# Performance work log

Measured on AMD Instinct MI355X. Metric: run time of the kernel, lower is better.

The kernel has to match this reference:

```python
import jax, jax.numpy as jnp
import numpy as np

COMMIT_W = 0.25
ENT_W = 0.1
ENT_T = 0.01
EPS = 1e-5


def setup_inputs() -> dict:
    key = jax.random.key(0)
    kx, kc = jax.random.split(key)
    x = jax.random.normal(kx, (32, 32, 32, 256), dtype=jnp.float32)
    # variance_scaling(1.0, fan_in, uniform) -> U(-sqrt(3/fan_in), sqrt(3/fan_in)), fan_in = 256
    lim = float(np.sqrt(3.0 / 256.0))
    codebook = jax.random.uniform(kc, (1024, 256), dtype=jnp.float32, minval=-lim, maxval=lim)
    return {"x": x, "codebook": codebook}


def _cdist(flat, codebook):
    # Euclidean distance (with sqrt, as jnp.linalg.norm in the original),
    # computed via the expanded quadratic form to avoid the [N,K,D] intermediate.
    d2 = (jnp.sum(flat * flat, axis=-1, keepdims=True)
          + jnp.sum(codebook * codebook, axis=-1)[None, :]
          - 2.0 * (flat @ codebook.T))
    return jnp.sqrt(jnp.maximum(d2, 0.0))  # [N, K]


def reference(x, codebook):
    D = x.shape[-1]
    flat = x.reshape(-1, D)                      # [N, D]
    distances = _cdist(flat, codebook)           # [N, K]
    flat_indices = jnp.argmin(distances, axis=-1)  # [N]
    indices = flat_indices.reshape(x.shape[:-1])
    # one_hot(indices) @ codebook == gather
    quantized = codebook[flat_indices].reshape(x.shape)

    # optax.l2_loss = 0.5 * (pred - target)^2
    commit_loss = 0.5 * jnp.mean((x - jax.lax.stop_gradient(quantized)) ** 2) * COMMIT_W
    codebook_loss = 0.5 * jnp.mean((jax.lax.stop_gradient(x) - quantized) ** 2)

    # entropy loss on affinity = -distances
    logits = (-distances) / ENT_T                # [N, K]
    probs = jax.nn.softmax(logits, axis=-1)
    log_probs = jax.nn.log_softmax(logits + EPS, axis=-1)
    avg_probs = jnp.mean(probs, axis=0)          # [K]
    avg_entropy = -jnp.sum(avg_probs * jnp.log(avg_probs + EPS))
    sample_entropy = -jnp.mean(jnp.sum(probs * log_probs, axis=-1))
    entropy_loss = (sample_entropy - avg_entropy) * ENT_W

    vq_loss = codebook_loss + commit_loss + entropy_loss
    # straight-through estimator
    quantized_st = x + jax.lax.stop_gradient(quantized - x)
    return quantized_st, vq_loss, commit_loss, codebook_loss, entropy_loss, indices
```

## Files before the change

### kernel.cpp

```cpp
#include <hip/hip_runtime.h>

#define N_ROWS 32768
#define DIMS 256
#define K_CODES 1024
#define MT 64
#define NCHUNK 256
#define KC 16
#define SA 68
#define SB 260

static constexpr size_t SC_OFF  = 8388608;
static constexpr size_t IDX_OFF = 8388612;

__device__ inline float wsum64(float v){
  #pragma unroll
  for(int off=32; off; off>>=1) v += __shfl_xor(v, off, 64);
  return v;
}

__global__ __launch_bounds__(256) void rowsq_np512_kernel(const float* __restrict__ X,
                                                          const float* __restrict__ CB,
                                                          float* __restrict__ xsq,
                                                          float* __restrict__ csq){
  const int t = threadIdx.x;
  const int wv = t >> 6, l = t & 63;
  const int sub = l >> 4, li = l & 15;
  #pragma unroll
  for(int p=0; p<4; p++){
    int r = blockIdx.x*64 + p*16 + wv*4 + sub;
    const float* s0; float* dst;
    if(r < K_CODES){ s0 = CB + (size_t)r*DIMS; dst = csq + r; }
    else { s0 = X + (size_t)(r - K_CODES)*DIMS; dst = xsq + (r - K_CODES); }
    float blk[2];
    #pragma unroll
    for(int bb=0; bb<2; bb++){
      float q[8];
      #pragma unroll
      for(int j=0;j<8;j++){
        float a = s0[bb*128 + j*16 + li];
        q[j] = __fmul_rn(a, a);
      }
      float v = __fadd_rn(__fadd_rn(__fadd_rn(q[0],q[1]), __fadd_rn(q[2],q[3])),
                          __fadd_rn(__fadd_rn(q[4],q[5]), __fadd_rn(q[6],q[7])));
      v = __fadd_rn(v, __shfl_xor(v, 8, 64));
      v = __fadd_rn(v, __shfl_xor(v, 4, 64));
      v = __fadd_rn(v, __shfl_xor(v, 2, 64));
      v = __fadd_rn(v, __shfl_xor(v, 1, 64));
      blk[bb] = v;
    }
    if(li == 0) *dst = __fadd_rn(blk[0], blk[1]);
  }
}

__global__ __launch_bounds__(256,2) void fused_argmin_kernel(
    const float* __restrict__ X, const float* __restrict__ CB,
    const float* __restrict__ xsq, const float* __restrict__ csq,
    float* __restrict__ hist, float* __restrict__ acc_sc,
    float* __restrict__ out)
{
  __shared__ __align__(16) float As[KC][SA];
  __shared__ __align__(16) float Bs[KC][SB];
  __shared__ __align__(16) float cs_lds[K_CODES];
  __shared__ __align__(16) float xs_lds[MT];
  __shared__ __align__(16) float4 cstat[4][MT];
  __shared__ int sk[MT];
  const int t  = threadIdx.x;
  const int tx = t & 31, ty = t >> 5;
  const int m0 = blockIdx.x * MT;

  reinterpret_cast<float4*>(cs_lds)[t] = reinterpret_cast<const float4*>(csq)[t];
  if(t < 16)
    reinterpret_cast<float4*>(xs_lds)[t] = reinterpret_cast<const float4*>(xsq + m0)[t];

  const int arow = t >> 2;
  const int acol = (t & 3) * 4;
  const float* Ag = X + (size_t)(m0 + arow)*DIMS + acol;

  float4 a4p, b4p[4];
  a4p = *(const float4*)(Ag);
  {
    const float* Bg = CB + (size_t)t*DIMS;
    #pragma unroll
    for(int q=0;q<4;q++) b4p[q] = *(const float4*)(Bg + q*4);
  }
  __syncthreads();

  float xs_[8];
  { float4 x0 = *(const float4*)&xs_lds[ty*8];
    float4 x1 = *(const float4*)&xs_lds[ty*8+4];
    xs_[0]=x0.x; xs_[1]=x0.y; xs_[2]=x0.z; xs_[3]=x0.w;
    xs_[4]=x1.x; xs_[5]=x1.y; xs_[6]=x1.z; xs_[7]=x1.w; }

  for(int nc=0; nc<4; nc++){
    const int n0c = nc*NCHUNK;
    float acc[8][8];
    #pragma unroll
    for(int i=0;i<8;i++)
      #pragma unroll
      for(int j=0;j<8;j++) acc[i][j]=0.f;

    for(int kc=0;kc<16;kc++){
      __syncthreads();
      As[acol+0][arow]=a4p.x; As[acol+1][arow]=a4p.y;
      As[acol+2][arow]=a4p.z; As[acol+3][arow]=a4p.w;
      #pragma unroll
      for(int q=0;q<4;q++){
        Bs[q*4+0][t]=b4p[q].x; Bs[q*4+1][t]=b4p[q].y;
        Bs[q*4+2][t]=b4p[q].z; Bs[q*4+3][t]=b4p[q].w;
      }
      __syncthreads();
      {
        int nkc = kc+1, nnc = nc;
        if(nkc==16){ nkc=0; nnc=(nc+1)&3; }
        const float* An = Ag + nkc*KC;
        const float* Bn = CB + (size_t)(nnc*NCHUNK + t)*DIMS + nkc*KC;
        a4p = *(const float4*)(An);
        #pragma unroll
        for(int q=0;q<4;q++) b4p[q]=*(const float4*)(Bn + q*4);
      }
      #pragma unroll
      for(int k=0;k<KC;k++){
        float4 a0 = *(const float4*)&As[k][ty*8];
        float4 a1 = *(const float4*)&As[k][ty*8+4];
        float4 b0 = *(const float4*)&Bs[k][tx*4];
        float4 b1 = *(const float4*)&Bs[k][128 + tx*4];
        float a_[8]={a0.x,a0.y,a0.z,a0.w, a1.x,a1.y,a1.z,a1.w};
        float b_[8]={b0.x,b0.y,b0.z,b0.w, b1.x,b1.y,b1.z,b1.w};
        #pragma unroll
        for(int r=0;r<8;r++)
          #pragma unroll
          for(int j=0;j<8;j++)
            acc[r][j] = fmaf(a_[r], b_[j], acc[r][j]);
      }
    }

    float csv[8];
    { float4 c0 = *(const float4*)&cs_lds[n0c + tx*4];
      float4 c1 = *(const float4*)&cs_lds[n0c + 128 + tx*4];
      csv[0]=c0.x; csv[1]=c0.y; csv[2]=c0.z; csv[3]=c0.w;
      csv[4]=c1.x; csv[5]=c1.y; csv[6]=c1.z; csv[7]=c1.w; }
    #pragma unroll
    for(int i=0;i<8;i++){
      float xs = xs_[i];
      float d[8];
      #pragma unroll
      for(int j=0;j<8;j++){
        float d2 = (xs + csv[j]) - 2.0f*acc[i][j];
        d[j] = sqrtf(fmaxf(d2, 0.f));
      }
      float dl = INFINITY; int kl = 0;
      #pragma unroll
      for(int j=0;j<8;j++){
        int kidx = n0c + (j>>2)*128 + tx*4 + (j&3);
        if(d[j] < dl){ dl = d[j]; kl = kidx; }
      }
      #pragma unroll
      for(int off=1; off<32; off<<=1){
        float od = __shfl_xor(dl, off, 64);
        int   ok = __shfl_xor(kl, off, 64);
        if(od < dl || (od == dl && ok < kl)){ dl = od; kl = ok; }
      }
      float s1=0.f, t2s=0.f;
      #pragma unroll
      for(int j=0;j<8;j++){
        float l = (dl - d[j])*100.0f;
        float e = expf(l);
        s1 += e; t2s = fmaf(e, l, t2s);
      }
      #pragma unroll
      for(int off=1; off<32; off<<=1){
        s1  += __shfl_xor(s1,  off, 64);
        t2s += __shfl_xor(t2s, off, 64);
      }
      if(tx == 0)
        cstat[nc][ty*8 + i] = make_float4(dl, __int_as_float(kl), s1, t2s);
    }
  }

  __syncthreads();
  float plogp = 0.f;
  if(t < MT){
    float4 c0 = cstat[0][t];
    float dm = c0.x; int km = __float_as_int(c0.y);
    float Ss = c0.z; float Ts = c0.w;
    #pragma unroll
    for(int nc=1; nc<4; nc++){
      float4 cn = cstat[nc][t];
      float dl = cn.x; int kl = __float_as_int(cn.y);
      float s1 = cn.z, t2s = cn.w;
      if(dl < dm){
        float del = 100.0f*(dl - dm); float al = expf(del);
        Ts = al*(Ts + Ss*del) + t2s;
        Ss = al*Ss + s1;
        dm = dl; km = kl;
      } else {
        float del = 100.0f*(dm - dl); float al = expf(del);
        Ts += al*(t2s + s1*del);
        Ss += al*s1;
      }
    }
    int n = m0 + t;
    out[IDX_OFF + n] = (float)km;
    sk[t] = km;
    atomicAdd(hist + km, 1.0f);
    plogp = Ts/Ss - logf(Ss);
  }
  plogp = wsum64(plogp);
  if((t & 63) == 0) atomicAdd(acc_sc + 1, plogp);

  __syncthreads();
  {
    int w = t>>6, lane = t&63;
    int row0 = w*16;
    float mse = 0.f;
    for(int r=0;r<16;r++){
      int n = m0 + row0 + r;
      int k = sk[row0 + r];
      float4 cb4 = *(const float4*)(CB + (size_t)k*DIMS + lane*4);
      float4 x4  = *(const float4*)(X  + (size_t)n*DIMS + lane*4);
      float e0=x4.x-cb4.x, e1=x4.y-cb4.y, e2=x4.z-cb4.z, e3=x4.w-cb4.w;
      mse += e0*e0 + e1*e1 + e2*e2 + e3*e3;
      *reinterpret_cast<float4*>(out + (size_t)n*DIMS + lane*4) = cb4;
    }
    mse = wsum64(mse);
    if(lane==0) atomicAdd(acc_sc+0, mse);
  }
}

__global__ __launch_bounds__(256) void finalize_kernel(const float* __restrict__ hist,
                                                       const float* __restrict__ acc_sc,
                                                       float* __restrict__ out){
  __shared__ float red[256];
  int t = threadIdx.x;
  float s = 0.f;
  #pragma unroll
  for(int c=0;c<4;c++){
    float ap = hist[c*256 + t] * (1.0f/32768.0f);
    s += ap * logf(ap + 1e-5f);
  }
  red[t] = s; __syncthreads();
  for(int off=128; off; off>>=1){
    if(t<off) red[t]+=red[t+off];
    __syncthreads();
  }
  if(t==0){
    float avg_entropy    = -red[0];
    float mse            = acc_sc[0] * (1.0f/8388608.0f);
    float sample_entropy = -(acc_sc[1] * (1.0f/32768.0f));
    float commit = 0.5f*mse*0.25f;
    float cbl    = 0.5f*mse;
    float ent    = (sample_entropy - avg_entropy)*0.1f;
    float vq     = cbl + commit + ent;
    out[SC_OFF+0] = vq;
    out[SC_OFF+1] = commit;
    out[SC_OFF+2] = cbl;
    out[SC_OFF+3] = ent;
  }
}

extern "C" void kernel_launch(void* const* d_in, const int* in_sizes, int n_in,
                              void* d_out, int out_size, void* d_ws, size_t ws_size,
                              hipStream_t stream){
  const float* X  = (const float*)d_in[0];
  const float* CB = (const float*)d_in[1];
  float* out = (float*)d_out;
  float* xsq     = (float*)d_ws;
  float* csq     = xsq + N_ROWS;
  float* hist    = csq + K_CODES;
  float* acc_sc  = hist + K_CODES;

  hipMemsetAsync(hist, 0, (K_CODES+2)*sizeof(float), stream);
  rowsq_np512_kernel <<<(K_CODES+N_ROWS)/64, 256, 0, stream>>>(X, CB, xsq, csq);
  fused_argmin_kernel<<<N_ROWS/MT, 256, 0, stream>>>(X, CB, xsq, csq, hist, acc_sc, out);
  finalize_kernel    <<<1, 256, 0, stream>>>(hist, acc_sc, out);
}
```

Before: 367.1 us.

## Restructure argmin GEMM to 512 threads with double-buffered codebook tiles

The fused distance/argmin kernel moves to 512-thread blocks, each wave owning 8 rows and the full 512-code chunk. The A tile is no longer staged in LDS: each wave reads its rows straight from global memory as broadcast float2 loads. Codebook tiles are double-buffered in LDS so each k-step needs one barrier instead of two, and the per-chunk reduction now spans the full wave over two chunks instead of four. The direct global A loads and a launch bound of 4 blocks per CU on 512-thread blocks may add memory latency or register pressure.

New measurement: 490.9 us. +33.7%, slower.

```diff
diff --git a/kernel.cpp b/kernel.cpp
--- a/kernel.cpp
+++ b/kernel.cpp
@@ -4,10 +4,9 @@
 #define DIMS 256
 #define K_CODES 1024
 #define MT 64
-#define NCHUNK 256
+#define NCHUNK 512
 #define KC 16
-#define SA 68
-#define SB 260
+#define SBW 520
 
 static constexpr size_t SC_OFF  = 8388608;
 static constexpr size_t IDX_OFF = 8388612;
@@ -52,128 +51,129 @@
   }
 }
 
-__global__ __launch_bounds__(256,2) void fused_argmin_kernel(
+__global__ __launch_bounds__(512,4) void fused_argmin_kernel(
     const float* __restrict__ X, const float* __restrict__ CB,
     const float* __restrict__ xsq, const float* __restrict__ csq,
     float* __restrict__ hist, float* __restrict__ acc_sc,
     float* __restrict__ out)
 {
-  __shared__ __align__(16) float As[KC][SA];
-  __shared__ __align__(16) float Bs[KC][SB];
-  __shared__ __align__(16) float cs_lds[K_CODES];
-  __shared__ __align__(16) float xs_lds[MT];
-  __shared__ __align__(16) float4 cstat[4][MT];
+  __shared__ __align__(16) float Bs[2][KC][SBW];
+  __shared__ __align__(16) float4 cstat[2][MT];
   __shared__ int sk[MT];
   const int t  = threadIdx.x;
-  const int tx = t & 31, ty = t >> 5;
+  const int tx = t & 63;
+  const int wid = __builtin_amdgcn_readfirstlane(t >> 6);
   const int m0 = blockIdx.x * MT;
 
-  reinterpret_cast<float4*>(cs_lds)[t] = reinterpret_cast<const float4*>(csq)[t];
-  if(t < 16)
-    reinterpret_cast<float4*>(xs_lds)[t] = reinterpret_cast<const float4*>(xsq + m0)[t];
-
-  const int arow = t >> 2;
-  const int acol = (t & 3) * 4;
-  const float* Ag = X + (size_t)(m0 + arow)*DIMS + acol;
-
-  float4 a4p, b4p[4];
-  a4p = *(const float4*)(Ag);
+  const float* Aw = X + (size_t)(m0 + wid*8)*DIMS;
+
+  float xs_[8];
+  #pragma unroll
+  for(int i=0;i<8;i++) xs_[i] = xsq[m0 + wid*8 + i];
+
+  float4 b4p[4];
   {
     const float* Bg = CB + (size_t)t*DIMS;
     #pragma unroll
     for(int q=0;q<4;q++) b4p[q] = *(const float4*)(Bg + q*4);
   }
+  #pragma unroll
+  for(int q=0;q<4;q++){
+    Bs[0][q*4+0][t]=b4p[q].x; Bs[0][q*4+1][t]=b4p[q].y;
+    Bs[0][q*4+2][t]=b4p[q].z; Bs[0][q*4+3][t]=b4p[q].w;
+  }
   __syncthreads();
 
-  float xs_[8];
-  { float4 x0 = *(const float4*)&xs_lds[ty*8];
-    float4 x1 = *(const float4*)&xs_lds[ty*8+4];
-    xs_[0]=x0.x; xs_[1]=x0.y; xs_[2]=x0.z; xs_[3]=x0.w;
-    xs_[4]=x1.x; xs_[5]=x1.y; xs_[6]=x1.z; xs_[7]=x1.w; }
-
-  for(int nc=0; nc<4; nc++){
-    const int n0c = nc*NCHUNK;
-    float acc[8][8];
-    #pragma unroll
-    for(int i=0;i<8;i++)
-      #pragma unroll
-      for(int j=0;j<8;j++) acc[i][j]=0.f;
-
-    for(int kc=0;kc<16;kc++){
-      __syncthreads();
-      As[acol+0][arow]=a4p.x; As[acol+1][arow]=a4p.y;
-      As[acol+2][arow]=a4p.z; As[acol+3][arow]=a4p.w;
-      #pragma unroll
-      for(int q=0;q<4;q++){
-        Bs[q*4+0][t]=b4p[q].x; Bs[q*4+1][t]=b4p[q].y;
-        Bs[q*4+2][t]=b4p[q].z; Bs[q*4+3][t]=b4p[q].w;
-      }
-      __syncthreads();
-      {
-        int nkc = kc+1, nnc = nc;
-        if(nkc==16){ nkc=0; nnc=(nc+1)&3; }
-        const float* An = Ag + nkc*KC;
-        const float* Bn = CB + (size_t)(nnc*NCHUNK + t)*DIMS + nkc*KC;
-        a4p = *(const float4*)(An);
-        #pragma unroll
-        for(int q=0;q<4;q++) b4p[q]=*(const float4*)(Bn + q*4);
-      }
-      #pragma unroll
-      for(int k=0;k<KC;k++){
-        float4 a0 = *(const float4*)&As[k][ty*8];
-        float4 a1 = *(const float4*)&As[k][ty*8+4];
-        float4 b0 = *(const float4*)&Bs[k][tx*4];
-        float4 b1 = *(const float4*)&Bs[k][128 + tx*4];
-        float a_[8]={a0.x,a0.y,a0.z,a0.w, a1.x,a1.y,a1.z,a1.w};
+  float acc[8][8];
+  #pragma unroll
+  for(int i=0;i<8;i++)
+    #pragma unroll
+    for(int j=0;j<8;j++) acc[i][j]=0.f;
+
+  for(int s=0; s<32; s++){
+    const int cur = s & 1;
+    {
+      int s2 = (s+1) & 31;
+      const float* Bg = CB + (size_t)((s2>>4)*NCHUNK + t)*DIMS + (s2&15)*KC;
+      #pragma unroll
+      for(int q=0;q<4;q++) b4p[q] = *(const float4*)(Bg + q*4);
+    }
+    const int kb = (s&15)*KC;
+    #pragma unroll
+    for(int k2=0;k2<KC/2;k2++){
+      float2 a2[8];
+      #pragma unroll
+      for(int r=0;r<8;r++) a2[r] = *(const float2*)(Aw + r*DIMS + kb + k2*2);
+      #pragma unroll
+      for(int kk=0;kk<2;kk++){
+        const int k = k2*2 + kk;
+        float4 b0 = *(const float4*)&Bs[cur][k][tx*4];
+        float4 b1 = *(const float4*)&Bs[cur][k][256 + tx*4];
         float b_[8]={b0.x,b0.y,b0.z,b0.w, b1.x,b1.y,b1.z,b1.w};
         #pragma unroll
-        for(int r=0;r<8;r++)
+        for(int r=0;r<8;r++){
+          float av = kk ? a2[r].y : a2[r].x;
           #pragma unroll
           for(int j=0;j<8;j++)
-            acc[r][j] = fmaf(a_[r], b_[j], acc[r][j]);
-      }
-    }
-
-    float csv[8];
-    { float4 c0 = *(const float4*)&cs_lds[n0c + tx*4];
-      float4 c1 = *(const float4*)&cs_lds[n0c + 128 + tx*4];
-      csv[0]=c0.x; csv[1]=c0.y; csv[2]=c0.z; csv[3]=c0.w;
-      csv[4]=c1.x; csv[5]=c1.y; csv[6]=c1.z; csv[7]=c1.w; }
-    #pragma unroll
-    for(int i=0;i<8;i++){
-      float xs = xs_[i];
-      float d[8];
-      #pragma unroll
-      for(int j=0;j<8;j++){
-        float d2 = (xs + csv[j]) - 2.0f*acc[i][j];
-        d[j] = sqrtf(fmaxf(d2, 0.f));
-      }
-      float dl = INFINITY; int kl = 0;
-      #pragma unroll
-      for(int j=0;j<8;j++){
-        int kidx = n0c + (j>>2)*128 + tx*4 + (j&3);
-        if(d[j] < dl){ dl = d[j]; kl = kidx; }
-      }
-      #pragma unroll
-      for(int off=1; off<32; off<<=1){
-        float od = __shfl_xor(dl, off, 64);
-        int   ok = __shfl_xor(kl, off, 64);
-        if(od < dl || (od == dl && ok < kl)){ dl = od; kl = ok; }
-      }
-      float s1=0.f, t2s=0.f;
-      #pragma unroll
-      for(int j=0;j<8;j++){
-        float l = (dl - d[j])*100.0f;
-        float e = expf(l);
-        s1 += e; t2s = fmaf(e, l, t2s);
-      }
-      #pragma unroll
-      for(int off=1; off<32; off<<=1){
-        s1  += __shfl_xor(s1,  off, 64);
-        t2s += __shfl_xor(t2s, off, 64);
-      }
-      if(tx == 0)
-        cstat[nc][ty*8 + i] = make_float4(dl, __int_as_float(kl), s1, t2s);
+            acc[r][j] = fmaf(av, b_[j], acc[r][j]);
+        }
+      }
+    }
+    #pragma unroll
+    for(int q=0;q<4;q++){
+      Bs[cur^1][q*4+0][t]=b4p[q].x; Bs[cur^1][q*4+1][t]=b4p[q].y;
+      Bs[cur^1][q*4+2][t]=b4p[q].z; Bs[cur^1][q*4+3][t]=b4p[q].w;
+    }
+    __syncthreads();
+
+    if((s & 15) == 15){
+      const int nc = s >> 4;
+      const int n0c = nc * NCHUNK;
+      float csv[8];
+      { float4 c0 = *(const float4*)(csq + n0c + tx*4);
+        float4 c1 = *(const float4*)(csq + n0c + 256 + tx*4);
+        csv[0]=c0.x; csv[1]=c0.y; csv[2]=c0.z; csv[3]=c0.w;
+        csv[4]=c1.x; csv[5]=c1.y; csv[6]=c1.z; csv[7]=c1.w; }
+      #pragma unroll
+      for(int i=0;i<8;i++){
+        float xs = xs_[i];
+        float d[8];
+        #pragma unroll
+        for(int j=0;j<8;j++){
+          float d2 = (xs + csv[j]) - 2.0f*acc[i][j];
+          d[j] = sqrtf(fmaxf(d2, 0.f));
+        }
+        float dl = INFINITY; int kl = 0;
+        #pragma unroll
+        for(int j=0;j<8;j++){
+          int kidx = n0c + (j>>2)*256 + tx*4 + (j&3);
+          if(d[j] < dl){ dl = d[j]; kl = kidx; }
+        }
+        #pragma unroll
+        for(int off=1; off<64; off<<=1){
+          float od = __shfl_xor(dl, off, 64);
+          int   ok = __shfl_xor(kl, off, 64);
+          if(od < dl || (od == dl && ok < kl)){ dl = od; kl = ok; }
+        }
+        float s1=0.f, t2s=0.f;
+        #pragma unroll
+        for(int j=0;j<8;j++){
+          float l = (dl - d[j])*100.0f;
+          float e = expf(l);
+          s1 += e; t2s = fmaf(e, l, t2s);
+        }
+        #pragma unroll
+        for(int off=1; off<64; off<<=1){
+          s1  += __shfl_xor(s1,  off, 64);
+          t2s += __shfl_xor(t2s, off, 64);
+        }
+        if(tx == 0)
+          cstat[nc][wid*8 + i] = make_float4(dl, __int_as_float(kl), s1, t2s);
+      }
+      #pragma unroll
+      for(int i=0;i<8;i++)
+        #pragma unroll
+        for(int j=0;j<8;j++) acc[i][j]=0.f;
     }
   }
 
@@ -183,9 +183,8 @@
     float4 c0 = cstat[0][t];
     float dm = c0.x; int km = __float_as_int(c0.y);
     float Ss = c0.z; float Ts = c0.w;
-    #pragma unroll
-    for(int nc=1; nc<4; nc++){
-      float4 cn = cstat[nc][t];
+    {
+      float4 cn = cstat[1][t];
       float dl = cn.x; int kl = __float_as_int(cn.y);
       float s1 = cn.z, t2s = cn.w;
       if(dl < dm){
@@ -210,10 +209,11 @@
 
   __syncthreads();
   {
-    int w = t>>6, lane = t&63;
-    int row0 = w*16;
+    int lane = t & 63;
+    int row0 = wid*8;
     float mse = 0.f;
-    for(int r=0;r<16;r++){
+    #pragma unroll
+    for(int r=0;r<8;r++){
       int n = m0 + row0 + r;
       int k = sk[row0 + r];
       float4 cb4 = *(const float4*)(CB + (size_t)k*DIMS + lane*4);
@@ -271,6 +271,6 @@
 
   hipMemsetAsync(hist, 0, (K_CODES+2)*sizeof(float), stream);
   rowsq_np512_kernel <<<(K_CODES+N_ROWS)/64, 256, 0, stream>>>(X, CB, xsq, csq);
-  fused_argmin_kernel<<<N_ROWS/MT, 256, 0, stream>>>(X, CB, xsq, csq, hist, acc_sc, out);
+  fused_argmin_kernel<<<N_ROWS/MT, 512, 0, stream>>>(X, CB, xsq, csq, hist, acc_sc, out);
   finalize_kernel    <<<1, 256, 0, stream>>>(hist, acc_sc, out);
 }
```
